# Kernel tuning notes

Hardware: AMD Instinct MI355X
Metric: run time of the kernel (lower is better)

Reference implementation:

```python
import jax, jax.numpy as jnp
import numpy as np

DIM = 384
H_RES, W_RES = 56, 56
HEADS = 12
WS = 7          # window size
SS = 3          # shift size
N = WS * WS     # tokens per window
NW = (H_RES // WS) * (W_RES // WS)
EPS = 1e-5


def _rel_pos_index(ws):
    coords = np.stack(np.meshgrid(np.arange(ws), np.arange(ws), indexing='ij'))  # [2,ws,ws]
    cf = coords.reshape(2, -1)                      # [2, N]
    rc = (cf[:, :, None] - cf[:, None, :]).transpose(1, 2, 0)  # [N,N,2]
    rc[..., 0] += ws - 1
    rc[..., 1] += ws - 1
    rc[..., 0] *= 2 * ws - 1
    return rc.sum(-1)                               # [N,N] int


def _attn_mask(h, w, ws, ss):
    img = np.zeros((h, w))
    cnt = 0
    slices = (slice(0, -ws), slice(-ws, -ss), slice(-ss, None))
    for hs in slices:
        for wsl in slices:
            img[hs, wsl] = cnt
            cnt += 1
    mw = img.reshape(h // ws, ws, w // ws, ws).transpose(0, 2, 1, 3).reshape(-1, ws * ws)  # [nW,N]
    d = mw[:, None, :] - mw[:, :, None]
    return np.where(d != 0, -100.0, 0.0).astype(np.float32)  # [nW,N,N]


RPI = jnp.asarray(_rel_pos_index(WS).reshape(-1))          # [N*N]
ATTN_MASK = jnp.asarray(_attn_mask(H_RES, W_RES, WS, SS))  # [nW,N,N]


def _layernorm(x, g, b):
    mu = jnp.mean(x, axis=-1, keepdims=True)
    var = jnp.mean(jnp.square(x - mu), axis=-1, keepdims=True)
    return (x - mu) * jax.lax.rsqrt(var + EPS) * g + b


def setup_inputs() -> dict:
    key = jax.random.key(0)
    ks = jax.random.split(key, 8)
    s = 0.02
    return {
        'x': jax.random.normal(ks[0], (32, 1 + H_RES * W_RES, DIM), jnp.float32),
        'norm1_g': jnp.ones((DIM,), jnp.float32),
        'norm1_b': jnp.zeros((DIM,), jnp.float32),
        'qkv_w': jax.random.normal(ks[1], (DIM, 3 * DIM), jnp.float32) * s,
        'qkv_b': jnp.zeros((3 * DIM,), jnp.float32),
        'rpb_table': jax.random.normal(ks[2], ((2 * WS - 1) ** 2, HEADS), jnp.float32) * s,
        'proj_w': jax.random.normal(ks[3], (DIM, DIM), jnp.float32) * s,
        'proj_b': jnp.zeros((DIM,), jnp.float32),
        'norm2_g': jnp.ones((DIM,), jnp.float32),
        'norm2_b': jnp.zeros((DIM,), jnp.float32),
        'fc1_w': jax.random.normal(ks[4], (DIM, 4 * DIM), jnp.float32) * s,
        'fc1_b': jnp.zeros((4 * DIM,), jnp.float32),
        'fc2_w': jax.random.normal(ks[5], (4 * DIM, DIM), jnp.float32) * s,
        'fc2_b': jnp.zeros((DIM,), jnp.float32),
    }


def reference(x, norm1_g, norm1_b, qkv_w, qkv_b, rpb_table, proj_w, proj_b,
              norm2_g, norm2_b, fc1_w, fc1_b, fc2_w, fc2_b):
    B = x.shape[0]
    C = DIM
    hd = C // HEADS
    scale = hd ** -0.5

    time_token = x[:, :1, :]          # [B,1,C]
    img = x[:, 1:, :]                 # [B,H*W,C]
    shortcut = img

    h = _layernorm(img, norm1_g, norm1_b).reshape(B, H_RES, W_RES, C)
    h = jnp.roll(h, shift=(-SS, -SS), axis=(1, 2))  # cyclic shift

    # window partition -> [B*nW, N, C]
    xw = h.reshape(B, H_RES // WS, WS, W_RES // WS, WS, C)
    xw = xw.transpose(0, 1, 3, 2, 4, 5).reshape(-1, N, C)

    # window attention
    qkv = (xw @ qkv_w + qkv_b).reshape(-1, N, 3, HEADS, hd).transpose(2, 0, 3, 1, 4)
    q, k, v = qkv[0], qkv[1], qkv[2]                 # [B*nW, H, N, hd]
    attn = jnp.einsum('whnd,whmd->whnm', q * scale, k)
    bias = rpb_table[RPI].reshape(N, N, HEADS).transpose(2, 0, 1)  # [H,N,N]
    attn = attn + bias[None]
    attn = attn.reshape(B, NW, HEADS, N, N) + ATTN_MASK[None, :, None]
    attn = jax.nn.softmax(attn.reshape(-1, HEADS, N, N), axis=-1)
    out = jnp.einsum('whnm,whmd->wnhd', attn, v).reshape(-1, N, C)
    out = out @ proj_w + proj_b

    # window reverse -> [B,H,W,C]
    out = out.reshape(B, H_RES // WS, W_RES // WS, WS, WS, C)
    out = out.transpose(0, 1, 3, 2, 4, 5).reshape(B, H_RES, W_RES, C)
    out = jnp.roll(out, shift=(SS, SS), axis=(1, 2)).reshape(B, H_RES * W_RES, C)

    img = shortcut + out
    x = jnp.concatenate([time_token, img], axis=1)   # [B,1+H*W,C]
    x = _layernorm(x, norm2_g, norm2_b)
    hmlp = jax.nn.gelu(x @ fc1_w + fc1_b, approximate=False)
    x = x + (hmlp @ fc2_w + fc2_b)
    return x
```

## Files before the change

kernel.cpp:

```cpp
#include <hip/hip_runtime.h>
#include <hip/hip_bf16.h>

#define DIM 384
#define HEADS 12
#define NTOK 49
#define TOKENS 3137
#define M_ATTN 100352
#define M_FULL 100384
#define M_PAD  100480
#define SCALEQ 0.17677669529663687f

typedef __attribute__((ext_vector_type(8))) short s8v;
typedef __attribute__((ext_vector_type(4))) float f4v;
typedef unsigned short u16;

__device__ __forceinline__ float b2f(int s) {
  union { unsigned u; float f; } c; c.u = ((unsigned)(s & 0xffff)) << 16; return c.f;
}
__device__ __forceinline__ u16 f2b(float f) {
  __hip_bfloat16 h = __float2bfloat16(f);
  return *reinterpret_cast<u16*>(&h);
}
__device__ __forceinline__ void gload16(const void* g, void* l) {
  __builtin_amdgcn_global_load_lds((const __attribute__((address_space(1))) void*)g,
                                   (__attribute__((address_space(3))) void*)l, 16, 0, 0);
}

__global__ void k_convert(const float* __restrict__ qkv_w, const float* __restrict__ qkv_b,
                          const float* __restrict__ proj_w, const float* __restrict__ fc1_w,
                          const float* __restrict__ fc2_w,
                          u16* __restrict__ wt_qkv, float* __restrict__ qkvb_s,
                          u16* __restrict__ wt_proj, u16* __restrict__ wt_fc1,
                          u16* __restrict__ wt_fc2) {
  int i = blockIdx.x * 256 + threadIdx.x;
  if (i < 1152 * 384) { int n = i / 384, k = i % 384;
    float v = qkv_w[(size_t)k * 1152 + n]; if (n < 384) v *= SCALEQ; wt_qkv[i] = f2b(v); }
  if (i < 1152) qkvb_s[i] = qkv_b[i] * (i < 384 ? SCALEQ : 1.0f);
  if (i < 384 * 384) { int n = i / 384, k = i % 384; wt_proj[i] = f2b(proj_w[(size_t)k * 384 + n]); }
  if (i < 1536 * 384) { int n = i / 384, k = i % 384; wt_fc1[i] = f2b(fc1_w[(size_t)k * 1536 + n]); }
  if (i < 384 * 1536) { int n = i / 1536, k = i % 1536; wt_fc2[i] = f2b(fc2_w[(size_t)k * 384 + n]); }
}

__global__ void k_addtab(const float* __restrict__ rpb, float* __restrict__ ADD) {
  int idx = blockIdx.x * 256 + threadIdx.x;
  if (idx >= 4 * HEADS * NTOK * NTOK) return;
  int j = idx % NTOK, t = idx / NTOK;
  int i = t % NTOK; t /= NTOK;
  int h = t % HEADS; int cls = t / HEADS;
  int ii = i / 7, jj = i % 7, ji = j / 7, j2 = j % 7;
  int rpi = (ii - ji + 6) * 13 + (jj - j2 + 6);
  float v = rpb[rpi * HEADS + h];
  int rh = (cls & 2) ? (ii < 4 ? 1 : 2) : 0;
  int rw = (cls & 1) ? (jj < 4 ? 1 : 2) : 0;
  int sh = (cls & 2) ? (ji < 4 ? 1 : 2) : 0;
  int sw = (cls & 1) ? (j2 < 4 ? 1 : 2) : 0;
  if (rh != sh || rw != sw) v -= 100.0f;
  ADD[idx] = v;
}

__global__ void k_ln1(const float* __restrict__ x, const float* __restrict__ g,
                      const float* __restrict__ b, u16* __restrict__ xw, int t0) {
  int wid = threadIdx.x >> 6, lane = threadIdx.x & 63;
  int t = t0 + blockIdx.x * 4 + wid;
  int bi = t / 3136, rem = t % 3136;
  int win = rem / NTOK, n = rem % NTOK;
  int wh = win >> 3, ww = win & 7, ii = n / 7, jj = n % 7;
  int h = (wh * 7 + ii + 3) % 56;
  int w = (ww * 7 + jj + 3) % 56;
  const float* src = x + ((size_t)bi * TOKENS + 1 + h * 56 + w) * DIM;
  float v[6];
  #pragma unroll
  for (int e = 0; e < 6; e++) v[e] = src[lane + e * 64];
  float s = v[0] + v[1] + v[2] + v[3] + v[4] + v[5];
  #pragma unroll
  for (int m = 1; m < 64; m <<= 1) s += __shfl_xor(s, m);
  float mu = s * (1.0f / 384.0f);
  float q = 0.f;
  #pragma unroll
  for (int e = 0; e < 6; e++) { float d = v[e] - mu; q += d * d; }
  #pragma unroll
  for (int m = 1; m < 64; m <<= 1) q += __shfl_xor(q, m);
  float rstd = rsqrtf(q * (1.0f / 384.0f) + 1e-5f);
  u16* dst = xw + (size_t)(t - t0) * DIM;
  #pragma unroll
  for (int e = 0; e < 6; e++) {
    int c = lane + e * 64;
    dst[c] = f2b((v[e] - mu) * rstd * g[c] + b[c]);
  }
}

template<int MODE>
__global__ __launch_bounds__(256) void k_gemm(
    const u16* __restrict__ A, const u16* __restrict__ Bt,
    const float* __restrict__ bias, u16* __restrict__ Cb,
    float* __restrict__ outp, const u16* __restrict__ resid,
    int N, int K, int row_off) {
  __shared__ __align__(16) u16 As[128 * 64];
  __shared__ __align__(16) u16 Bs[128 * 64];
  int t = threadIdx.x;
  int m0 = blockIdx.y * 128, n0 = blockIdx.x * 128;
  int lane = t & 63, wave = t >> 6;
  int lo = lane & 15, hi = lane >> 4;
  int wr = (wave >> 1) * 64, wc = (wave & 1) * 64;
  int rl = lane >> 3;
  int sl = (lane & 7) ^ rl;
  const u16* Ag = A + (size_t)(m0 + wave * 32 + rl) * K + sl * 8;
  const u16* Bg = Bt + (size_t)(n0 + wave * 32 + rl) * K + sl * 8;
  u16* Al = As + (wave * 32) * 64;
  u16* Bl = Bs + (wave * 32) * 64;
  f4v acc[4][4];
  #pragma unroll
  for (int m = 0; m < 4; m++)
    #pragma unroll
    for (int n = 0; n < 4; n++) acc[m][n] = (f4v)(0.0f);
  for (int kt = 0; kt < K; kt += 64) {
    __syncthreads();
    #pragma unroll
    for (int g = 0; g < 4; g++) {
      gload16(Ag + (size_t)(g * 8) * K + kt, Al + g * 8 * 64);
      gload16(Bg + (size_t)(g * 8) * K + kt, Bl + g * 8 * 64);
    }
    __syncthreads();
    #pragma unroll
    for (int kk = 0; kk < 2; kk++) {
      s8v af[4], bfr[4];
      #pragma unroll
      for (int m = 0; m < 4; m++) {
        int row = wr + m * 16 + lo;
        af[m] = *(const s8v*)(As + row * 64 + (((kk * 4 + hi) ^ (row & 7)) * 8));
      }
      #pragma unroll
      for (int n = 0; n < 4; n++) {
        int row = wc + n * 16 + lo;
        bfr[n] = *(const s8v*)(Bs + row * 64 + (((kk * 4 + hi) ^ (row & 7)) * 8));
      }
      #pragma unroll
      for (int m = 0; m < 4; m++)
        #pragma unroll
        for (int n = 0; n < 4; n++)
          acc[m][n] = __builtin_amdgcn_mfma_f32_16x16x32_bf16(af[m], bfr[n], acc[m][n], 0, 0, 0);
    }
  }
  #pragma unroll
  for (int m = 0; m < 4; m++) {
    int grow = m0 + wr + m * 16 + hi * 4;
    #pragma unroll
    for (int n = 0; n < 4; n++) {
      int gcol = n0 + wc + n * 16 + lo;
      float bv = bias[gcol];
      #pragma unroll
      for (int r = 0; r < 4; r++) {
        float val = acc[m][n][r] + bv;
        size_t idx = (size_t)(grow + r) * N + gcol;
        if (MODE == 0) {
          Cb[idx] = f2b(val);
        } else if (MODE == 1) {
          float u = __builtin_fmaf(0.0713548163f * val, val * val, 1.5957691216f * val);
          float gl = val * __builtin_amdgcn_rcpf(1.0f + __expf(-u));
          Cb[idx] = f2b(gl);
        } else {
          int orow = grow + r + row_off;
          if (orow < M_FULL) {
            size_t oi = (size_t)orow * DIM + gcol;
            outp[oi] = val + b2f(resid[oi]);
          }
        }
      }
    }
  }
}

__global__ __launch_bounds__(256) void k_attn2(const u16* __restrict__ qkv,
                                               const float* __restrict__ ADD,
                                               u16* __restrict__ ao, int win0) {
  __shared__ u16 PT[4][64][76];
  __shared__ u16 VT[4][32][76];
  int wid = threadIdx.x >> 6, lane = threadIdx.x & 63;
  int lo = lane & 15, hi = lane >> 4;
  int win_l = blockIdx.x * 4 + wid;
  int nw = (win0 + win_l) & 63;
  int wh = nw >> 3, ww = nw & 7;
  int cls = ((wh == 7) ? 2 : 0) + ((ww == 7) ? 1 : 0);
  size_t rowbase = (size_t)win_l * NTOK;
  u16 (*pt)[76] = PT[wid];
  u16 (*vt)[76] = VT[wid];

  int rcl[4];
  #pragma unroll
  for (int ti = 0; ti < 4; ti++) {
    int r = ti * 16 + lo;
    rcl[ti] = r < NTOK ? r : NTOK - 1;
  }
  int jrow = lane < NTOK ? lane : NTOK - 1;

  for (int h = 0; h < HEADS; h++) {
    s8v af[4], bf[4];
    #pragma unroll
    for (int ti = 0; ti < 4; ti++) {
      af[ti] = *(const s8v*)(qkv + (rowbase + rcl[ti]) * 1152 + h * 32 + hi * 8);
      bf[ti] = *(const s8v*)(qkv + (rowbase + rcl[ti]) * 1152 + 384 + h * 32 + hi * 8);
    }
    f4v st[4][4];
    #pragma unroll
    for (int mi = 0; mi < 4; mi++)
      #pragma unroll
      for (int ni = 0; ni < 4; ni++)
        st[mi][ni] = __builtin_amdgcn_mfma_f32_16x16x32_bf16(af[mi], bf[ni], (f4v)(0.0f), 0, 0, 0);

    {
      const u16* vsrc = qkv + (rowbase + jrow) * 1152 + 768 + h * 32;
      #pragma unroll
      for (int d0 = 0; d0 < 32; d0 += 8) {
        s8v v = *(const s8v*)(vsrc + d0);
        #pragma unroll
        for (int e = 0; e < 8; e++) vt[d0 + e][lane] = (u16)v[e];
      }
    }

    const float* addb = ADD + ((size_t)cls * HEADS + h) * (NTOK * NTOK);
    #pragma unroll
    for (int mi = 0; mi < 4; mi++)
      #pragma unroll
      for (int ni = 0; ni < 4; ni++) {
        int jj = ni * 16 + lo;
        #pragma unroll
        for (int r = 0; r < 4; r++) {
          int i = mi * 16 + hi * 4 + r;
          if (jj < NTOK) {
            int ic = i < NTOK ? i : NTOK - 1;
            st[mi][ni][r] += addb[ic * NTOK + jj];
          } else st[mi][ni][r] = -1e30f;
        }
      }

    float invl[4][4];
    #pragma unroll
    for (int mi = 0; mi < 4; mi++)
      #pragma unroll
      for (int r = 0; r < 4; r++) {
        float m = fmaxf(fmaxf(st[mi][0][r], st[mi][1][r]), fmaxf(st[mi][2][r], st[mi][3][r]));
        #pragma unroll
        for (int msk = 1; msk < 16; msk <<= 1) m = fmaxf(m, __shfl_xor(m, msk));
        float s = 0.f;
        #pragma unroll
        for (int ni = 0; ni < 4; ni++) {
          float p = __expf(st[mi][ni][r] - m);
          st[mi][ni][r] = p;
          s += p;
        }
        #pragma unroll
        for (int msk = 1; msk < 16; msk <<= 1) s += __shfl_xor(s, msk);
        invl[mi][r] = 1.0f / s;
      }

    #pragma unroll
    for (int ni = 0; ni < 4; ni++)
      #pragma unroll
      for (int mi = 0; mi < 4; mi++) {
        ushort4 pk;
        pk.x = f2b(st[mi][ni][0]); pk.y = f2b(st[mi][ni][1]);
        pk.z = f2b(st[mi][ni][2]); pk.w = f2b(st[mi][ni][3]);
        *(ushort4*)(&pt[ni * 16 + lo][mi * 16 + hi * 4]) = pk;
      }

    f4v ot[4][2];
    #pragma unroll
    for (int mi = 0; mi < 4; mi++)
      #pragma unroll
      for (int dt = 0; dt < 2; dt++) ot[mi][dt] = (f4v)(0.0f);
    #pragma unroll
    for (int kt = 0; kt < 2; kt++) {
      s8v pa[4], vb[2];
      #pragma unroll
      for (int mi = 0; mi < 4; mi++) {
        s8v p;
        #pragma unroll
        for (int e = 0; e < 8; e++) p[e] = (short)pt[kt * 32 + hi * 8 + e][mi * 16 + lo];
        pa[mi] = p;
      }
      #pragma unroll
      for (int dt = 0; dt < 2; dt++) {
        short4 a = *(const short4*)(&vt[dt * 16 + lo][kt * 32 + hi * 8]);
        short4 b = *(const short4*)(&vt[dt * 16 + lo][kt * 32 + hi * 8 + 4]);
        s8v v; v[0] = a.x; v[1] = a.y; v[2] = a.z; v[3] = a.w;
               v[4] = b.x; v[5] = b.y; v[6] = b.z; v[7] = b.w;
        vb[dt] = v;
      }
      #pragma unroll
      for (int mi = 0; mi < 4; mi++)
        #pragma unroll
        for (int dt = 0; dt < 2; dt++)
          ot[mi][dt] = __builtin_amdgcn_mfma_f32_16x16x32_bf16(pa[mi], vb[dt], ot[mi][dt], 0, 0, 0);
    }

    #pragma unroll
    for (int mi = 0; mi < 4; mi++)
      #pragma unroll
      for (int r = 0; r < 4; r++) {
        int i = mi * 16 + hi * 4 + r;
        if (i < NTOK) {
          u16* op = ao + (rowbase + i) * DIM + h * 32 + lo;
          op[0]  = f2b(ot[mi][0][r] * invl[mi][r]);
          op[16] = f2b(ot[mi][1][r] * invl[mi][r]);
        }
      }
  }
}

__global__ void k_ln2(const float* __restrict__ x, const u16* __restrict__ proj,
                      const float* __restrict__ g, const float* __restrict__ b,
                      u16* __restrict__ x2b) {
  int wid = threadIdx.x >> 6, lane = threadIdx.x & 63;
  int r = blockIdx.x * 4 + wid;
  u16* dst = x2b + (size_t)r * DIM;
  if (r >= M_FULL) {
    u16 z = f2b(0.0f);
    #pragma unroll
    for (int e = 0; e < 6; e++) dst[lane + e * 64] = z;
    return;
  }
  int bi = r / TOKENS, tk = r % TOKENS;
  const float* xs = x + (size_t)r * DIM;
  float v[6];
  if (tk == 0) {
    #pragma unroll
    for (int e = 0; e < 6; e++) v[e] = xs[lane + e * 64];
  } else {
    int p = tk - 1, hh = p / 56, wp = p % 56;
    int a = (hh + 53) % 56, bw = (wp + 53) % 56;
    int wh = a / 7, ii = a % 7, w2 = bw / 7, jj = bw % 7;
    size_t prow = ((size_t)bi * 64 + wh * 8 + w2) * NTOK + ii * 7 + jj;
    const u16* ps = proj + prow * DIM;
    #pragma unroll
    for (int e = 0; e < 6; e++) v[e] = xs[lane + e * 64] + b2f(ps[lane + e * 64]);
  }
  float s = v[0] + v[1] + v[2] + v[3] + v[4] + v[5];
  #pragma unroll
  for (int m = 1; m < 64; m <<= 1) s += __shfl_xor(s, m);
  float mu = s * (1.0f / 384.0f);
  float q = 0.f;
  #pragma unroll
  for (int e = 0; e < 6; e++) { float d = v[e] - mu; q += d * d; }
  #pragma unroll
  for (int m = 1; m < 64; m <<= 1) q += __shfl_xor(q, m);
  float rstd = rsqrtf(q * (1.0f / 384.0f) + 1e-5f);
  #pragma unroll
  for (int e = 0; e < 6; e++) {
    int c = lane + e * 64;
    dst[c] = f2b((v[e] - mu) * rstd * g[c] + b[c]);
  }
}

extern "C" void kernel_launch(void* const* d_in, const int* in_sizes, int n_in,
                              void* d_out, int out_size, void* d_ws, size_t ws_size,
                              hipStream_t stream) {
  const float* x      = (const float*)d_in[0];
  const float* n1g    = (const float*)d_in[1];
  const float* n1b    = (const float*)d_in[2];
  const float* qkv_w  = (const float*)d_in[3];
  const float* qkv_b  = (const float*)d_in[4];
  const float* rpb    = (const float*)d_in[5];
  const float* proj_w = (const float*)d_in[6];
  const float* proj_b = (const float*)d_in[7];
  const float* n2g    = (const float*)d_in[8];
  const float* n2b    = (const float*)d_in[9];
  const float* fc1_w  = (const float*)d_in[10];
  const float* fc1_b  = (const float*)d_in[11];
  const float* fc2_w  = (const float*)d_in[12];
  const float* fc2_b  = (const float*)d_in[13];
  float* outp = (float*)d_out;

  auto al = [](size_t v) { return (v + 255) & ~(size_t)255; };
  const int cand[8][2] = {{1,1},{1,2},{2,2},{2,4},{4,4},{4,8},{8,8},{16,16}};
  int NC1 = 16, NC2 = 16;
  for (int ci = 0; ci < 8; ci++) {
    int c1 = cand[ci][0], c2 = cand[ci][1];
    int cbb = (785 + c2 - 1) / c2;
    size_t tot = al(884736) + al(294912) + al(1179648) + al(1179648) + al(4608)
               + al(460992)
               + al((size_t)(M_ATTN / c1) * 768)
               + al((size_t)(M_ATTN / c1) * 2304)
               + al((size_t)M_ATTN * 768)
               + al((size_t)M_PAD * 768)
               + al((size_t)cbb * 128 * 1536 * 2);
    if (tot <= ws_size) { NC1 = c1; NC2 = c2; break; }
  }
  char* p = (char*)d_ws;
  auto take = [&](size_t bytes) { char* r = p; p += al(bytes); return r; };
  u16* wt_qkv  = (u16*)take(884736);
  u16* wt_proj = (u16*)take(294912);
  u16* wt_fc1  = (u16*)take(1179648);
  u16* wt_fc2  = (u16*)take(1179648);
  float* qkvb_s = (float*)take(4608);
  float* ADDt   = (float*)take(460992);
  int chunkM = M_ATTN / NC1;
  u16* XW   = (u16*)take((size_t)chunkM * 768);
  u16* QKV  = (u16*)take((size_t)chunkM * 2304);
  u16* PROJ = (u16*)take((size_t)M_ATTN * 768);
  u16* X2B  = (u16*)take((size_t)M_PAD * 768);
  int cb = (785 + NC2 - 1) / NC2;
  u16* FC1  = (u16*)take((size_t)cb * 128 * 1536 * 2);
  u16* AO = XW;

  k_convert<<<2304, 256, 0, stream>>>(qkv_w, qkv_b, proj_w, fc1_w, fc2_w,
                                      wt_qkv, qkvb_s, wt_proj, wt_fc1, wt_fc2);
  k_addtab<<<451, 256, 0, stream>>>(rpb, ADDt);
  int chunkWin = chunkM / NTOK;
  for (int c = 0; c < NC1; c++) {
    int t0 = c * chunkM;
    k_ln1<<<chunkM / 4, 256, 0, stream>>>(x, n1g, n1b, XW, t0);
    k_gemm<0><<<dim3(9, chunkM / 128), 256, 0, stream>>>(XW, wt_qkv, qkvb_s, QKV,
                                                         nullptr, nullptr, 1152, 384, 0);
    k_attn2<<<chunkWin / 4, 256, 0, stream>>>(QKV, ADDt, AO, c * chunkWin);
    k_gemm<0><<<dim3(3, chunkM / 128), 256, 0, stream>>>(AO, wt_proj, proj_b,
                                                         PROJ + (size_t)t0 * DIM,
                                                         nullptr, nullptr, 384, 384, 0);
  }
  k_ln2<<<M_PAD / 4, 256, 0, stream>>>(x, PROJ, n2g, n2b, X2B);
  for (int c = 0; c < NC2; c++) {
    int rb0 = c * cb;
    int nb = 785 - rb0; if (nb > cb) nb = cb; if (nb <= 0) break;
    k_gemm<1><<<dim3(12, nb), 256, 0, stream>>>(X2B + (size_t)rb0 * 128 * DIM, wt_fc1,
                                                fc1_b, FC1, nullptr, nullptr, 1536, 384, 0);
    k_gemm<2><<<dim3(3, nb), 256, 0, stream>>>(FC1, wt_fc2, fc2_b, nullptr, outp, X2B,
                                               384, 1536, rb0 * 128);
  }
}
```

Baseline: 1.013 ms.

## Double-buffer GEMM LDS tiles and remap blocks for XCD locality

Switches the bf16 MFMA GEMM to two LDS buffers, so the global-to-LDS load of the next K tile is issued before the current tile's fragments are read and multiplied. Explicit vmcnt/lgkmcnt waits, barriers and raised wave priority around the MFMA block keep the stages ordered. It also remaps the linear workgroup id so that consecutive tiles land on the same XCD, which improves L2 reuse of A and B rows. LDS use doubles to 64KB per block, which may cut occupancy.

```diff
diff --git a/kernel.cpp b/kernel.cpp
--- a/kernel.cpp
+++ b/kernel.cpp
@@ -95,10 +95,16 @@
     const float* __restrict__ bias, u16* __restrict__ Cb,
     float* __restrict__ outp, const u16* __restrict__ resid,
     int N, int K, int row_off) {
-  __shared__ __align__(16) u16 As[128 * 64];
-  __shared__ __align__(16) u16 Bs[128 * 64];
+  __shared__ __align__(16) u16 As[2][128 * 64];
+  __shared__ __align__(16) u16 Bs[2][128 * 64];
+  int gx = gridDim.x;
+  int lid = blockIdx.y * gx + blockIdx.x;
+  int nwg = gx * gridDim.y;
+  int q = nwg >> 3, r = nwg & 7;
+  int xcd = lid & 7, loc = lid >> 3;
+  int tile = (xcd < r ? xcd * (q + 1) : r * (q + 1) + (xcd - r) * q) + loc;
+  int m0 = (tile / gx) * 128, n0 = (tile % gx) * 128;
   int t = threadIdx.x;
-  int m0 = blockIdx.y * 128, n0 = blockIdx.x * 128;
   int lane = t & 63, wave = t >> 6;
   int lo = lane & 15, hi = lane >> 4;
   int wr = (wave >> 1) * 64, wc = (wave & 1) * 64;
@@ -106,41 +112,60 @@
   int sl = (lane & 7) ^ rl;
   const u16* Ag = A + (size_t)(m0 + wave * 32 + rl) * K + sl * 8;
   const u16* Bg = Bt + (size_t)(n0 + wave * 32 + rl) * K + sl * 8;
-  u16* Al = As + (wave * 32) * 64;
-  u16* Bl = Bs + (wave * 32) * 64;
   f4v acc[4][4];
   #pragma unroll
   for (int m = 0; m < 4; m++)
     #pragma unroll
     for (int n = 0; n < 4; n++) acc[m][n] = (f4v)(0.0f);
-  for (int kt = 0; kt < K; kt += 64) {
-    __syncthreads();
-    #pragma unroll
-    for (int g = 0; g < 4; g++) {
-      gload16(Ag + (size_t)(g * 8) * K + kt, Al + g * 8 * 64);
-      gload16(Bg + (size_t)(g * 8) * K + kt, Bl + g * 8 * 64);
-    }
-    __syncthreads();
+  int nt = K >> 6;
+#define STAGE(buf, kt) do {                                              \
+    u16* al_ = As[buf] + wave * 32 * 64;                                 \
+    u16* bl_ = Bs[buf] + wave * 32 * 64;                                 \
+    _Pragma("unroll")                                                    \
+    for (int g_ = 0; g_ < 4; g_++) {                                     \
+      gload16(Ag + (size_t)(g_ * 8) * K + (kt), al_ + g_ * 8 * 64);      \
+      gload16(Bg + (size_t)(g_ * 8) * K + (kt), bl_ + g_ * 8 * 64);      \
+    } } while (0)
+  STAGE(0, 0);
+  for (int kt = 0; kt < nt; ++kt) {
+    int c = kt & 1;
+    if (kt + 1 < nt) {
+      STAGE(1 - c, (kt + 1) << 6);
+      asm volatile("s_waitcnt vmcnt(8)" ::: "memory");
+    } else {
+      asm volatile("s_waitcnt vmcnt(0)" ::: "memory");
+    }
+    __builtin_amdgcn_s_barrier();
+    __builtin_amdgcn_sched_barrier(0);
+    s8v af[2][4], bfr[2][4];
     #pragma unroll
     for (int kk = 0; kk < 2; kk++) {
-      s8v af[4], bfr[4];
       #pragma unroll
       for (int m = 0; m < 4; m++) {
         int row = wr + m * 16 + lo;
-        af[m] = *(const s8v*)(As + row * 64 + (((kk * 4 + hi) ^ (row & 7)) * 8));
+        af[kk][m] = *(const s8v*)(As[c] + row * 64 + (((kk * 4 + hi) ^ (row & 7)) * 8));
       }
       #pragma unroll
       for (int n = 0; n < 4; n++) {
         int row = wc + n * 16 + lo;
-        bfr[n] = *(const s8v*)(Bs + row * 64 + (((kk * 4 + hi) ^ (row & 7)) * 8));
-      }
+        bfr[kk][n] = *(const s8v*)(Bs[c] + row * 64 + (((kk * 4 + hi) ^ (row & 7)) * 8));
+      }
+    }
+    asm volatile("s_waitcnt lgkmcnt(0)" ::: "memory");
+    __builtin_amdgcn_sched_barrier(0);
+    __builtin_amdgcn_s_barrier();
+    __builtin_amdgcn_sched_barrier(0);
+    __builtin_amdgcn_s_setprio(1);
+    #pragma unroll
+    for (int kk = 0; kk < 2; kk++)
       #pragma unroll
       for (int m = 0; m < 4; m++)
         #pragma unroll
         for (int n = 0; n < 4; n++)
-          acc[m][n] = __builtin_amdgcn_mfma_f32_16x16x32_bf16(af[m], bfr[n], acc[m][n], 0, 0, 0);
-    }
-  }
+          acc[m][n] = __builtin_amdgcn_mfma_f32_16x16x32_bf16(af[kk][m], bfr[kk][n], acc[m][n], 0, 0, 0);
+    __builtin_amdgcn_s_setprio(0);
+  }
+#undef STAGE
   #pragma unroll
   for (int m = 0; m < 4; m++) {
     int grow = m0 + wr + m * 16 + hi * 4;
@@ -149,9 +174,9 @@
       int gcol = n0 + wc + n * 16 + lo;
       float bv = bias[gcol];
       #pragma unroll
-      for (int r = 0; r < 4; r++) {
-        float val = acc[m][n][r] + bv;
-        size_t idx = (size_t)(grow + r) * N + gcol;
+      for (int r2 = 0; r2 < 4; r2++) {
+        float val = acc[m][n][r2] + bv;
+        size_t idx = (size_t)(grow + r2) * N + gcol;
         if (MODE == 0) {
           Cb[idx] = f2b(val);
         } else if (MODE == 1) {
@@ -159,7 +184,7 @@
           float gl = val * __builtin_amdgcn_rcpf(1.0f + __expf(-u));
           Cb[idx] = f2b(gl);
         } else {
-          int orow = grow + r + row_off;
+          int orow = grow + r2 + row_off;
           if (orow < M_FULL) {
             size_t oi = (size_t)orow * DIM + gcol;
             outp[oi] = val + b2f(resid[oi]);
```

New measurement: 1.007 ms. No clear change (-0.5%).

## Fuse MLP fc1+GELU+fc2 into one panel kernel with resident activation rows

Applied to the files above, without the earlier changes.

Replaces the generic tiled GEMM with a row-panel kernel that keeps a 128x384 activation block in LDS and streams weight tiles past it. For the MLP, the GELU hidden chunk stays in LDS and is fed straight into fc2, so the large FC1 intermediate is never written to or read back from global memory, and the residual comes from the resident panel. The QKV and proj GEMMs also use the panel kernel. In exchange there are far fewer blocks (785 for the MLP, about 784 for the others), one block per CU at high LDS use, and each weight stage waits on its load with no double buffering, so latency may be exposed.

```diff
diff --git a/kernel.cpp b/kernel.cpp
--- a/kernel.cpp
+++ b/kernel.cpp
@@ -24,6 +24,10 @@
 __device__ __forceinline__ void gload16(const void* g, void* l) {
   __builtin_amdgcn_global_load_lds((const __attribute__((address_space(1))) void*)g,
                                    (__attribute__((address_space(3))) void*)l, 16, 0, 0);
+}
+__device__ __forceinline__ float gelu_f(float val) {
+  float u = __builtin_fmaf(0.0713548163f * val, val * val, 1.5957691216f * val);
+  return val * __builtin_amdgcn_rcpf(1.0f + __expf(-u));
 }
 
 __global__ void k_convert(const float* __restrict__ qkv_w, const float* __restrict__ qkv_b,
@@ -90,83 +94,185 @@
 }
 
 template<int MODE>
-__global__ __launch_bounds__(256) void k_gemm(
-    const u16* __restrict__ A, const u16* __restrict__ Bt,
-    const float* __restrict__ bias, u16* __restrict__ Cb,
-    float* __restrict__ outp, const u16* __restrict__ resid,
-    int N, int K, int row_off) {
-  __shared__ __align__(16) u16 As[128 * 64];
-  __shared__ __align__(16) u16 Bs[128 * 64];
-  int t = threadIdx.x;
-  int m0 = blockIdx.y * 128, n0 = blockIdx.x * 128;
-  int lane = t & 63, wave = t >> 6;
-  int lo = lane & 15, hi = lane >> 4;
-  int wr = (wave >> 1) * 64, wc = (wave & 1) * 64;
-  int rl = lane >> 3;
-  int sl = (lane & 7) ^ rl;
-  const u16* Ag = A + (size_t)(m0 + wave * 32 + rl) * K + sl * 8;
-  const u16* Bg = Bt + (size_t)(n0 + wave * 32 + rl) * K + sl * 8;
-  u16* Al = As + (wave * 32) * 64;
-  u16* Bl = Bs + (wave * 32) * 64;
-  f4v acc[4][4];
-  #pragma unroll
-  for (int m = 0; m < 4; m++)
-    #pragma unroll
-    for (int n = 0; n < 4; n++) acc[m][n] = (f4v)(0.0f);
-  for (int kt = 0; kt < K; kt += 64) {
-    __syncthreads();
-    #pragma unroll
-    for (int g = 0; g < 4; g++) {
-      gload16(Ag + (size_t)(g * 8) * K + kt, Al + g * 8 * 64);
-      gload16(Bg + (size_t)(g * 8) * K + kt, Bl + g * 8 * 64);
+__global__ __launch_bounds__(512, 1) void k_panel(
+    const u16* __restrict__ A, const u16* __restrict__ Wa, const u16* __restrict__ Wb,
+    const float* __restrict__ ba, const float* __restrict__ bb,
+    u16* __restrict__ outb, float* __restrict__ outf, int N) {
+  __shared__ __align__(16) u16 Xs[128 * 384];
+  __shared__ __align__(16) u16 Ws[128 * 64];
+  __shared__ __align__(16) u16 Hs[(MODE == 1) ? 128 * 128 : 16];
+  int tid = threadIdx.x;
+  int wid = tid >> 6, lane = tid & 63, lo = lane & 15, hi = lane >> 4;
+  int mh = (wid >> 2) * 64;
+  int nq = (wid & 3) * 32;
+  int m0 = blockIdx.x * 128;
+  const u16* Ap = A + (size_t)m0 * 384;
+
+  #pragma unroll
+  for (int i = 0; i < 12; i++) {
+    int f = (wid * 12 + i) * 1024 + lane * 16;
+    int row = f / 768;
+    int slot = (f - row * 768) >> 4;
+    gload16(Ap + row * 384 + ((slot ^ (row & 7)) << 3),
+            (char*)Xs + (wid * 12 + i) * 1024);
+  }
+
+  auto stageW = [&](const u16* Wt, int Krow, int rowbase, int kc) {
+    #pragma unroll
+    for (int i = 0; i < 2; i++) {
+      int f = (wid * 2 + i) * 1024 + lane * 16;
+      int row = f >> 7;
+      int slot = (f >> 4) & 7;
+      gload16(Wt + (size_t)(rowbase + row) * Krow + kc + ((slot ^ (row & 7)) << 3),
+              (char*)Ws + (wid * 2 + i) * 1024);
     }
-    __syncthreads();
-    #pragma unroll
-    for (int kk = 0; kk < 2; kk++) {
-      s8v af[4], bfr[4];
-      #pragma unroll
-      for (int m = 0; m < 4; m++) {
-        int row = wr + m * 16 + lo;
-        af[m] = *(const s8v*)(As + row * 64 + (((kk * 4 + hi) ^ (row & 7)) * 8));
-      }
-      #pragma unroll
-      for (int n = 0; n < 4; n++) {
-        int row = wc + n * 16 + lo;
-        bfr[n] = *(const s8v*)(Bs + row * 64 + (((kk * 4 + hi) ^ (row & 7)) * 8));
-      }
-      #pragma unroll
-      for (int m = 0; m < 4; m++)
-        #pragma unroll
-        for (int n = 0; n < 4; n++)
-          acc[m][n] = __builtin_amdgcn_mfma_f32_16x16x32_bf16(af[m], bfr[n], acc[m][n], 0, 0, 0);
+  };
+
+  if (MODE == 0) {
+    int nch = N >> 7;
+    for (int ch = 0; ch < nch; ch++) {
+      f4v acc[4][2];
+      #pragma unroll
+      for (int mi = 0; mi < 4; mi++)
+        #pragma unroll
+        for (int ni = 0; ni < 2; ni++) acc[mi][ni] = (f4v)(0.0f);
+      for (int ks = 0; ks < 6; ks++) {
+        __syncthreads();
+        stageW(Wa, 384, ch * 128, ks * 64);
+        asm volatile("s_waitcnt vmcnt(0)" ::: "memory");
+        __syncthreads();
+        #pragma unroll
+        for (int kk = 0; kk < 2; kk++) {
+          s8v a[4], b[2];
+          #pragma unroll
+          for (int mi = 0; mi < 4; mi++) {
+            int m = mh + mi * 16 + lo; int s = (ks * 2 + kk) * 4 + hi;
+            a[mi] = *(const s8v*)(Xs + m * 384 + ((s ^ (m & 7)) << 3));
+          }
+          #pragma unroll
+          for (int ni = 0; ni < 2; ni++) {
+            int nr = nq + ni * 16 + lo; int s = kk * 4 + hi;
+            b[ni] = *(const s8v*)(Ws + nr * 64 + ((s ^ (nr & 7)) << 3));
+          }
+          #pragma unroll
+          for (int mi = 0; mi < 4; mi++)
+            #pragma unroll
+            for (int ni = 0; ni < 2; ni++)
+              acc[mi][ni] = __builtin_amdgcn_mfma_f32_16x16x32_bf16(a[mi], b[ni], acc[mi][ni], 0, 0, 0);
+        }
+      }
+      #pragma unroll
+      for (int mi = 0; mi < 4; mi++)
+        #pragma unroll
+        for (int ni = 0; ni < 2; ni++) {
+          int gcol = ch * 128 + nq + ni * 16 + lo;
+          float bv = ba[gcol];
+          #pragma unroll
+          for (int r = 0; r < 4; r++) {
+            int grow = mh + mi * 16 + hi * 4 + r;
+            outb[(size_t)(m0 + grow) * N + gcol] = f2b(acc[mi][ni][r] + bv);
+          }
+        }
     }
-  }
-  #pragma unroll
-  for (int m = 0; m < 4; m++) {
-    int grow = m0 + wr + m * 16 + hi * 4;
-    #pragma unroll
-    for (int n = 0; n < 4; n++) {
-      int gcol = n0 + wc + n * 16 + lo;
-      float bv = bias[gcol];
-      #pragma unroll
-      for (int r = 0; r < 4; r++) {
-        float val = acc[m][n][r] + bv;
-        size_t idx = (size_t)(grow + r) * N + gcol;
-        if (MODE == 0) {
-          Cb[idx] = f2b(val);
-        } else if (MODE == 1) {
-          float u = __builtin_fmaf(0.0713548163f * val, val * val, 1.5957691216f * val);
-          float gl = val * __builtin_amdgcn_rcpf(1.0f + __expf(-u));
-          Cb[idx] = f2b(gl);
-        } else {
-          int orow = grow + r + row_off;
-          if (orow < M_FULL) {
-            size_t oi = (size_t)orow * DIM + gcol;
-            outp[oi] = val + b2f(resid[oi]);
-          }
-        }
-      }
+  } else {
+    f4v acc2[3][4][2];
+    #pragma unroll
+    for (int g = 0; g < 3; g++)
+      #pragma unroll
+      for (int mi = 0; mi < 4; mi++)
+        #pragma unroll
+        for (int ni = 0; ni < 2; ni++) acc2[g][mi][ni] = (f4v)(0.0f);
+    for (int ch = 0; ch < 12; ch++) {
+      f4v acc1[4][2];
+      #pragma unroll
+      for (int mi = 0; mi < 4; mi++)
+        #pragma unroll
+        for (int ni = 0; ni < 2; ni++) acc1[mi][ni] = (f4v)(0.0f);
+      for (int ks = 0; ks < 6; ks++) {
+        __syncthreads();
+        stageW(Wa, 384, ch * 128, ks * 64);
+        asm volatile("s_waitcnt vmcnt(0)" ::: "memory");
+        __syncthreads();
+        #pragma unroll
+        for (int kk = 0; kk < 2; kk++) {
+          s8v a[4], b[2];
+          #pragma unroll
+          for (int mi = 0; mi < 4; mi++) {
+            int m = mh + mi * 16 + lo; int s = (ks * 2 + kk) * 4 + hi;
+            a[mi] = *(const s8v*)(Xs + m * 384 + ((s ^ (m & 7)) << 3));
+          }
+          #pragma unroll
+          for (int ni = 0; ni < 2; ni++) {
+            int nr = nq + ni * 16 + lo; int s = kk * 4 + hi;
+            b[ni] = *(const s8v*)(Ws + nr * 64 + ((s ^ (nr & 7)) << 3));
+          }
+          #pragma unroll
+          for (int mi = 0; mi < 4; mi++)
+            #pragma unroll
+            for (int ni = 0; ni < 2; ni++)
+              acc1[mi][ni] = __builtin_amdgcn_mfma_f32_16x16x32_bf16(a[mi], b[ni], acc1[mi][ni], 0, 0, 0);
+        }
+      }
+      #pragma unroll
+      for (int mi = 0; mi < 4; mi++)
+        #pragma unroll
+        for (int ni = 0; ni < 2; ni++) {
+          int col = nq + ni * 16 + lo;
+          float bv = ba[ch * 128 + col];
+          int sl = col >> 3, el = col & 7;
+          #pragma unroll
+          for (int r = 0; r < 4; r++) {
+            int m = mh + mi * 16 + hi * 4 + r;
+            Hs[m * 128 + ((sl ^ (m & 7)) << 3) + el] = f2b(gelu_f(acc1[mi][ni][r] + bv));
+          }
+        }
+      #pragma unroll
+      for (int n2g = 0; n2g < 3; n2g++)
+        for (int kt2 = 0; kt2 < 2; kt2++) {
+          __syncthreads();
+          stageW(Wb, 1536, n2g * 128, ch * 128 + kt2 * 64);
+          asm volatile("s_waitcnt vmcnt(0)" ::: "memory");
+          __syncthreads();
+          #pragma unroll
+          for (int kk = 0; kk < 2; kk++) {
+            s8v a[4], b[2];
+            #pragma unroll
+            for (int mi = 0; mi < 4; mi++) {
+              int m = mh + mi * 16 + lo; int s = (kt2 * 2 + kk) * 4 + hi;
+              a[mi] = *(const s8v*)(Hs + m * 128 + ((s ^ (m & 7)) << 3));
+            }
+            #pragma unroll
+            for (int ni = 0; ni < 2; ni++) {
+              int nr = nq + ni * 16 + lo; int s = kk * 4 + hi;
+              b[ni] = *(const s8v*)(Ws + nr * 64 + ((s ^ (nr & 7)) << 3));
+            }
+            #pragma unroll
+            for (int mi = 0; mi < 4; mi++)
+              #pragma unroll
+              for (int ni = 0; ni < 2; ni++)
+                acc2[n2g][mi][ni] = __builtin_amdgcn_mfma_f32_16x16x32_bf16(a[mi], b[ni], acc2[n2g][mi][ni], 0, 0, 0);
+          }
+        }
     }
+    #pragma unroll
+    for (int n2g = 0; n2g < 3; n2g++)
+      #pragma unroll
+      for (int mi = 0; mi < 4; mi++)
+        #pragma unroll
+        for (int ni = 0; ni < 2; ni++) {
+          int gcol = n2g * 128 + nq + ni * 16 + lo;
+          float bv = bb[gcol];
+          int sl = gcol >> 3, el = gcol & 7;
+          #pragma unroll
+          for (int r = 0; r < 4; r++) {
+            int ml = mh + mi * 16 + hi * 4 + r;
+            int orow = m0 + ml;
+            if (orow < M_FULL) {
+              float res = b2f(Xs[ml * 384 + ((sl ^ (ml & 7)) << 3) + el]);
+              outf[(size_t)orow * 384 + gcol] = acc2[n2g][mi][ni][r] + bv + res;
+            }
+          }
+        }
   }
 }
 
@@ -371,19 +477,14 @@
   float* outp = (float*)d_out;
 
   auto al = [](size_t v) { return (v + 255) & ~(size_t)255; };
-  const int cand[8][2] = {{1,1},{1,2},{2,2},{2,4},{4,4},{4,8},{8,8},{16,16}};
-  int NC1 = 16, NC2 = 16;
-  for (int ci = 0; ci < 8; ci++) {
-    int c1 = cand[ci][0], c2 = cand[ci][1];
-    int cbb = (785 + c2 - 1) / c2;
-    size_t tot = al(884736) + al(294912) + al(1179648) + al(1179648) + al(4608)
-               + al(460992)
-               + al((size_t)(M_ATTN / c1) * 768)
-               + al((size_t)(M_ATTN / c1) * 2304)
-               + al((size_t)M_ATTN * 768)
-               + al((size_t)M_PAD * 768)
-               + al((size_t)cbb * 128 * 1536 * 2);
-    if (tot <= ws_size) { NC1 = c1; NC2 = c2; break; }
+  size_t fixed = al(884736) + al(294912) + al(1179648) + al(1179648) + al(4608)
+               + al(460992) + al((size_t)M_ATTN * 768) + al((size_t)M_PAD * 768);
+  const int cands[5] = {1, 2, 4, 8, 16};
+  int NC1 = 16;
+  for (int ci = 0; ci < 5; ci++) {
+    int c1 = cands[ci];
+    size_t tot = fixed + al((size_t)(M_ATTN / c1) * 768) + al((size_t)(M_ATTN / c1) * 2304);
+    if (tot <= ws_size) { NC1 = c1; break; }
   }
   char* p = (char*)d_ws;
   auto take = [&](size_t bytes) { char* r = p; p += al(bytes); return r; };
@@ -393,13 +494,11 @@
   u16* wt_fc2  = (u16*)take(1179648);
   float* qkvb_s = (float*)take(4608);
   float* ADDt   = (float*)take(460992);
+  u16* PROJ = (u16*)take((size_t)M_ATTN * 768);
+  u16* X2B  = (u16*)take((size_t)M_PAD * 768);
   int chunkM = M_ATTN / NC1;
   u16* XW   = (u16*)take((size_t)chunkM * 768);
   u16* QKV  = (u16*)take((size_t)chunkM * 2304);
-  u16* PROJ = (u16*)take((size_t)M_ATTN * 768);
-  u16* X2B  = (u16*)take((size_t)M_PAD * 768);
-  int cb = (785 + NC2 - 1) / NC2;
-  u16* FC1  = (u16*)take((size_t)cb * 128 * 1536 * 2);
   u16* AO = XW;
 
   k_convert<<<2304, 256, 0, stream>>>(qkv_w, qkv_b, proj_w, fc1_w, fc2_w,
@@ -409,20 +508,13 @@
   for (int c = 0; c < NC1; c++) {
     int t0 = c * chunkM;
     k_ln1<<<chunkM / 4, 256, 0, stream>>>(x, n1g, n1b, XW, t0);
-    k_gemm<0><<<dim3(9, chunkM / 128), 256, 0, stream>>>(XW, wt_qkv, qkvb_s, QKV,
-                                                         nullptr, nullptr, 1152, 384, 0);
+    k_panel<0><<<chunkM / 128, 512, 0, stream>>>(XW, wt_qkv, nullptr, qkvb_s, nullptr,
+                                                 QKV, nullptr, 1152);
     k_attn2<<<chunkWin / 4, 256, 0, stream>>>(QKV, ADDt, AO, c * chunkWin);
-    k_gemm<0><<<dim3(3, chunkM / 128), 256, 0, stream>>>(AO, wt_proj, proj_b,
-                                                         PROJ + (size_t)t0 * DIM,
-                                                         nullptr, nullptr, 384, 384, 0);
+    k_panel<0><<<chunkM / 128, 512, 0, stream>>>(AO, wt_proj, nullptr, proj_b, nullptr,
+                                                 PROJ + (size_t)t0 * DIM, nullptr, 384);
   }
   k_ln2<<<M_PAD / 4, 256, 0, stream>>>(x, PROJ, n2g, n2b, X2B);
-  for (int c = 0; c < NC2; c++) {
-    int rb0 = c * cb;
-    int nb = 785 - rb0; if (nb > cb) nb = cb; if (nb <= 0) break;
-    k_gemm<1><<<dim3(12, nb), 256, 0, stream>>>(X2B + (size_t)rb0 * 128 * DIM, wt_fc1,
-                                                fc1_b, FC1, nullptr, nullptr, 1536, 384, 0);
-    k_gemm<2><<<dim3(3, nb), 256, 0, stream>>>(FC1, wt_fc2, fc2_b, nullptr, outp, X2B,
-                                               384, 1536, rb0 * 128);
-  }
-}
+  k_panel<1><<<M_PAD / 128, 512, 0, stream>>>(X2B, wt_fc1, wt_fc2, fc1_b, fc2_b,
+                                              nullptr, outp, 384);
+}
```

Result: slower. 1.258 ms (+24.2%).
